# Kernel tuning notes

Hardware: AMD Instinct MI355X
Metric: run time of the kernel (lower is better)

Reference implementation:

```python
import jax, jax.numpy as jnp
import numpy as np
import math

B, S, D, H = 4, 2048, 1024, 16
DK = D // H

def setup_inputs() -> dict:
    key = jax.random.key(0)
    ks = jax.random.split(key, 6)
    scale = 1.0 / math.sqrt(D)
    x = jax.random.normal(ks[0], (B, S, D), dtype=jnp.float32)
    mask = jnp.tril(jnp.ones((S, S), dtype=jnp.int32))[None, None]  # [1,1,S,S] causal
    Wq = jax.random.normal(ks[1], (D, D), dtype=jnp.float32) * scale
    Wk = jax.random.normal(ks[2], (D, D), dtype=jnp.float32) * scale
    Wv = jax.random.normal(ks[3], (D, D), dtype=jnp.float32) * scale
    Wo = jax.random.normal(ks[4], (D, D), dtype=jnp.float32) * scale
    z = jnp.zeros((D,), dtype=jnp.float32)
    return {"x": x, "mask": mask, "Wq": Wq, "bq": z, "Wk": Wk, "bk": z,
            "Wv": Wv, "bv": z, "Wo": Wo, "bo": z}

def reference(x, mask, Wq, bq, Wk, bk, Wv, bv, Wo, bo):
    bsz, seq_len, d_model = x.shape
    def split_heads(t):  # [B,S,D] -> [B,H,S,DK]
        return t.reshape(bsz, seq_len, H, DK).transpose(0, 2, 1, 3)
    Q = split_heads(x @ Wq + bq)
    K = split_heads(x @ Wk + bk)
    V = split_heads(x @ Wv + bv)
    scores = jnp.einsum('bhqd,bhkd->bhqk', Q, K) / jnp.sqrt(jnp.asarray(DK, x.dtype))
    scores = jnp.where(mask == 0, jnp.asarray(-jnp.inf, x.dtype), scores)
    attn = jax.nn.softmax(scores, axis=-1)
    # dropout is identity in eval mode
    context = jnp.einsum('bhqk,bhkd->bhqd', attn, V)
    context = context.transpose(0, 2, 1, 3).reshape(bsz, seq_len, d_model)
    return context @ Wo + bo
```

## Files before the change

### kernel.cpp

```cpp
#include <hip/hip_runtime.h>
#include <hip/hip_bf16.h>
#include <math.h>

#define BATCH 4
#define SEQ   2048
#define DMODEL 1024
#define NHEAD 16
#define DHEAD 64
#define MROWS (BATCH * SEQ)
#define SC_Q  0.1803368801111244f

typedef __attribute__((ext_vector_type(8))) short short8;
typedef __attribute__((ext_vector_type(4))) float f32x4;
typedef __attribute__((ext_vector_type(4))) unsigned short ushort4v;

__device__ inline unsigned short f2bf(float f) {
    union { float f; unsigned int u; } v; v.f = f;
    unsigned int r = v.u + 0x7FFFu + ((v.u >> 16) & 1u);
    return (unsigned short)(r >> 16);
}
__device__ inline unsigned short f2bf_fast(float f) {
    union { float f; unsigned int u; } v; v.f = f;
    return (unsigned short)((v.u + 0x8000u) >> 16);
}

__device__ __forceinline__ void g2l16(const unsigned short* g, unsigned short* l) {
    __builtin_amdgcn_global_load_lds(
        (const __attribute__((address_space(1))) unsigned int*)g,
        (__attribute__((address_space(3))) unsigned int*)l, 16, 0, 0);
}

__global__ __launch_bounds__(256) void cvt_bf16_kernel(
    const float* __restrict__ src, unsigned short* __restrict__ dst, int n4)
{
    const int i = blockIdx.x * 256 + threadIdx.x;
    if (i < n4) {
        float4 v = ((const float4*)src)[i];
        ushort4v o = { f2bf(v.x), f2bf(v.y), f2bf(v.z), f2bf(v.w) };
        ((ushort4v*)dst)[i] = o;
    }
}

__global__ __launch_bounds__(256) void bias_pack_kernel(
    const float* __restrict__ bq, const float* __restrict__ bk,
    const float* __restrict__ bv, float* __restrict__ b3)
{
    const int i = blockIdx.x * 256 + threadIdx.x;
    if (i < DMODEL) {
        b3[i]              = bq[i];
        b3[i + DMODEL]     = bk[i];
        b3[i + 2 * DMODEL] = bv[i];
    }
}

__global__ __launch_bounds__(256) void transpose_cvt_kernel(
    const float* __restrict__ W0, const float* __restrict__ W1,
    const float* __restrict__ W2, const float* __restrict__ W3,
    unsigned short* __restrict__ T0, unsigned short* __restrict__ T1,
    unsigned short* __restrict__ T2, unsigned short* __restrict__ T3)
{
    const float* W; unsigned short* T;
    switch (blockIdx.z) {
        case 0: W = W0; T = T0; break;
        case 1: W = W1; T = T1; break;
        case 2: W = W2; T = T2; break;
        default: W = W3; T = T3; break;
    }
    __shared__ float tile[32][33];
    const int r0 = blockIdx.y * 32, c0 = blockIdx.x * 32;
    const int c = threadIdx.x & 31, r = threadIdx.x >> 5;
    #pragma unroll
    for (int i = 0; i < 4; ++i)
        tile[r + i * 8][c] = W[(size_t)(r0 + r + i * 8) * DMODEL + c0 + c];
    __syncthreads();
    #pragma unroll
    for (int i = 0; i < 4; ++i)
        T[(size_t)(c0 + r + i * 8) * DMODEL + r0 + c] = f2bf(tile[c][r + i * 8]);
}

__global__ __launch_bounds__(256) void transpose_v_kernel(
    const unsigned short* __restrict__ Vin, unsigned short* __restrict__ Vt)
{
    __shared__ unsigned short t[64][72];
    const int tid = threadIdx.x;
    const int kt = blockIdx.x, bh = blockIdx.y;
    const unsigned short* src = Vin + ((size_t)bh * SEQ + kt * 64) * DHEAD;
    const int r = tid >> 3, c = (tid & 7) * 8;
    *(short8*)&t[r][c]      = *(const short8*)(src + (size_t)r * DHEAD + c);
    *(short8*)&t[r + 32][c] = *(const short8*)(src + (size_t)(r + 32) * DHEAD + c);
    __syncthreads();
    unsigned short* dst = Vt + (size_t)bh * DHEAD * SEQ + kt * 64;
    const int d = tid >> 3, k0 = (tid & 7) * 8;
    short8 v0, v1;
    #pragma unroll
    for (int i = 0; i < 8; ++i) {
        v0[i] = (short)t[k0 + i][d];
        v1[i] = (short)t[k0 + i][d + 32];
    }
    *(short8*)(dst + (size_t)d * SEQ + k0)        = v0;
    *(short8*)(dst + (size_t)(d + 32) * SEQ + k0) = v1;
}

__global__ __launch_bounds__(256) void gemm_qkv(
    const unsigned short* __restrict__ A, const unsigned short* __restrict__ Bt,
    const float* __restrict__ bias3, unsigned short* __restrict__ QKV )
{
    __shared__ unsigned short As[128 * 32];
    __shared__ unsigned short Bs[128 * 32];

    const int tid  = threadIdx.x;
    const int wave = tid >> 6, lane = tid & 63;
    const int l15  = lane & 15, quad = lane >> 4;
    const int wm   = (wave >> 1) * 64;
    const int wn   = (wave & 1) * 64;
    const int m0   = blockIdx.y * 128;
    const int n0   = blockIdx.x * 128;
    const int Kdim = DMODEL;

    f32x4 acc[4][4];
    #pragma unroll
    for (int i = 0; i < 4; ++i)
        #pragma unroll
        for (int j = 0; j < 4; ++j) acc[i][j] = (f32x4){0.f, 0.f, 0.f, 0.f};

    const int c_lo = wave * 64 + lane;

    for (int k0 = 0; k0 < Kdim; k0 += 32) {
        __syncthreads();
        {
            int c = c_lo;
            g2l16(A  + (size_t)(m0 + (c >> 2)) * Kdim + k0 + (c & 3) * 8, As + c * 8);
            g2l16(Bt + (size_t)(n0 + (c >> 2)) * Kdim + k0 + (c & 3) * 8, Bs + c * 8);
            c = c_lo + 256;
            g2l16(A  + (size_t)(m0 + (c >> 2)) * Kdim + k0 + (c & 3) * 8, As + c * 8);
            g2l16(Bt + (size_t)(n0 + (c >> 2)) * Kdim + k0 + (c & 3) * 8, Bs + c * 8);
        }
        __syncthreads();

        short8 af[4], bf[4];
        #pragma unroll
        for (int mi = 0; mi < 4; ++mi)
            af[mi] = *(const short8*)&As[(wm + mi * 16 + l15) * 32 + quad * 8];
        #pragma unroll
        for (int ni = 0; ni < 4; ++ni)
            bf[ni] = *(const short8*)&Bs[(wn + ni * 16 + l15) * 32 + quad * 8];
        #pragma unroll
        for (int mi = 0; mi < 4; ++mi)
            #pragma unroll
            for (int ni = 0; ni < 4; ++ni)
                acc[mi][ni] = __builtin_amdgcn_mfma_f32_16x16x32_bf16(
                    af[mi], bf[ni], acc[mi][ni], 0, 0, 0);
    }

    const size_t elems = (size_t)MROWS * DMODEL;
    #pragma unroll
    for (int mi = 0; mi < 4; ++mi) {
        #pragma unroll
        for (int r = 0; r < 4; ++r) {
            const int m = m0 + wm + mi * 16 + quad * 4 + r;
            const int b = m >> 11, s = m & 2047;
            #pragma unroll
            for (int ni = 0; ni < 4; ++ni) {
                const int n   = n0 + wn + ni * 16 + l15;
                const int seg = n >> 10, nn = n & 1023;
                const int h = nn >> 6, dk = nn & 63;
                const float sc  = (seg == 0) ? SC_Q : 1.0f;
                const float val = (acc[mi][ni][r] + bias3[n]) * sc;
                QKV[seg * elems + (((size_t)(b * NHEAD + h)) * SEQ + s) * DHEAD + dk] = f2bf(val);
            }
        }
    }
}

__global__ __launch_bounds__(256) void gemm_out(
    const unsigned short* __restrict__ A, const unsigned short* __restrict__ Bt,
    const float* __restrict__ bias, float* __restrict__ Cout)
{
    __shared__ unsigned short As[128 * 32];
    __shared__ unsigned short Bs[128 * 32];

    const int tid  = threadIdx.x;
    const int wave = tid >> 6, lane = tid & 63;
    const int l15  = lane & 15, quad = lane >> 4;
    const int wm   = (wave >> 1) * 64;
    const int wn   = (wave & 1) * 64;
    const int m0   = blockIdx.y * 128;
    const int n0   = blockIdx.x * 128;
    const int Kdim = DMODEL, Ndim = DMODEL;

    f32x4 acc[4][4];
    #pragma unroll
    for (int i = 0; i < 4; ++i)
        #pragma unroll
        for (int j = 0; j < 4; ++j) acc[i][j] = (f32x4){0.f, 0.f, 0.f, 0.f};

    const int c_lo = wave * 64 + lane;

    for (int k0 = 0; k0 < Kdim; k0 += 32) {
        __syncthreads();
        {
            int c = c_lo;
            g2l16(A  + (size_t)(m0 + (c >> 2)) * Kdim + k0 + (c & 3) * 8, As + c * 8);
            g2l16(Bt + (size_t)(n0 + (c >> 2)) * Kdim + k0 + (c & 3) * 8, Bs + c * 8);
            c = c_lo + 256;
            g2l16(A  + (size_t)(m0 + (c >> 2)) * Kdim + k0 + (c & 3) * 8, As + c * 8);
            g2l16(Bt + (size_t)(n0 + (c >> 2)) * Kdim + k0 + (c & 3) * 8, Bs + c * 8);
        }
        __syncthreads();

        short8 af[4], bf[4];
        #pragma unroll
        for (int mi = 0; mi < 4; ++mi)
            af[mi] = *(const short8*)&As[(wm + mi * 16 + l15) * 32 + quad * 8];
        #pragma unroll
        for (int ni = 0; ni < 4; ++ni)
            bf[ni] = *(const short8*)&Bs[(wn + ni * 16 + l15) * 32 + quad * 8];
        #pragma unroll
        for (int mi = 0; mi < 4; ++mi)
            #pragma unroll
            for (int ni = 0; ni < 4; ++ni)
                acc[mi][ni] = __builtin_amdgcn_mfma_f32_16x16x32_bf16(
                    af[mi], bf[ni], acc[mi][ni], 0, 0, 0);
    }

    #pragma unroll
    for (int mi = 0; mi < 4; ++mi) {
        #pragma unroll
        for (int r = 0; r < 4; ++r) {
            const int m = m0 + wm + mi * 16 + quad * 4 + r;
            #pragma unroll
            for (int ni = 0; ni < 4; ++ni) {
                const int n = n0 + wn + ni * 16 + l15;
                Cout[(size_t)m * Ndim + n] = acc[mi][ni][r] + bias[n];
            }
        }
    }
}

__global__ __launch_bounds__(256, 3) void attn_mfma4(
    const unsigned short* __restrict__ Q, const unsigned short* __restrict__ K,
    const unsigned short* __restrict__ VtG, unsigned short* __restrict__ ctx_out)
{
    __shared__ alignas(16) unsigned short Ks[64 * 64];
    __shared__ alignas(16) unsigned short Vts[64 * 64];
    __shared__ alignas(16) unsigned short Ps[4][32][72];

    const int tid  = threadIdx.x;
    const int wave = tid >> 6, lane = tid & 63;
    const int l15  = lane & 15, quad = lane >> 4;
    const int qa   = blockIdx.x;
    const int qb   = 31 - qa;
    const int bh   = blockIdx.y;
    const int b    = bh >> 4, h = bh & 15;

    const unsigned short* Kb0 = K   + (size_t)bh * SEQ * DHEAD;
    const unsigned short* Vb0 = VtG + (size_t)bh * DHEAD * SEQ;

    short8 qf[2][2];
    #pragma unroll
    for (int g = 0; g < 2; ++g) {
        const int qtile = g ? qb : qa;
        const unsigned short* qrow = Q + ((size_t)bh * SEQ + qtile * 64 + wave * 16 + l15) * DHEAD + quad * 8;
        qf[g][0] = *(const short8*)qrow;
        qf[g][1] = *(const short8*)(qrow + 32);
    }

    f32x4 Of[2][4];
    float l_r[2][4];
    #pragma unroll
    for (int g = 0; g < 2; ++g)
        #pragma unroll
        for (int i = 0; i < 4; ++i) { Of[g][i] = (f32x4){0.f,0.f,0.f,0.f}; l_r[g][i] = 0.f; }

    const int jb_end  = qb;
    const int row_loc = wave * 16 + quad * 4;
    const f32x4 zero4 = (f32x4){0.f, 0.f, 0.f, 0.f};

    const int c0c = wave * 64 + lane;
    short8 kreg[2], vreg[2];

    #pragma unroll
    for (int i = 0; i < 2; ++i) {
        const int c = c0c + i * 256;
        const int k = c >> 3, qs = c & 7;
        const int gq = qs ^ (k & 7);
        kreg[i] = *(const short8*)(Kb0 + (size_t)k * DHEAD + gq * 8);
        vreg[i] = *(const short8*)(Vb0 + (size_t)k * SEQ   + gq * 8);
    }

    for (int jb = 0; jb <= jb_end; ++jb) {
        __syncthreads();
        #pragma unroll
        for (int i = 0; i < 2; ++i) {
            const int c = c0c + i * 256;
            *(short8*)&Ks[c * 8]  = kreg[i];
            *(short8*)&Vts[c * 8] = vreg[i];
        }
        if (jb < jb_end) {
            const unsigned short* Kt  = Kb0 + (size_t)(jb + 1) * 64 * DHEAD;
            const unsigned short* Vt0 = Vb0 + (jb + 1) * 64;
            #pragma unroll
            for (int i = 0; i < 2; ++i) {
                const int c = c0c + i * 256;
                const int k = c >> 3, qs = c & 7;
                const int gq = qs ^ (k & 7);
                kreg[i] = *(const short8*)(Kt  + (size_t)k * DHEAD + gq * 8);
                vreg[i] = *(const short8*)(Vt0 + (size_t)k * SEQ   + gq * 8);
            }
        }
        __syncthreads();

        const bool act0  = (jb <= qa);
        const bool diag0 = (jb == qa);
        const bool diag1 = (jb == qb);

        #pragma unroll
        for (int nt = 0; nt < 4; ++nt) {
            const int k = nt * 16 + l15;
            short8 b0 = *(const short8*)&Ks[(k * 8 + ( quad      ^ (k & 7))) * 8];
            short8 b1 = *(const short8*)&Ks[(k * 8 + ((quad + 4) ^ (k & 7))) * 8];
            const int col = nt * 16 + l15;

            f32x4 s1 = __builtin_amdgcn_mfma_f32_16x16x32_bf16(qf[1][0], b0, zero4, 0, 0, 0);
            s1       = __builtin_amdgcn_mfma_f32_16x16x32_bf16(qf[1][1], b1, s1,    0, 0, 0);
            #pragma unroll
            for (int r = 0; r < 4; ++r) {
                float p = __builtin_amdgcn_exp2f(s1[r]);
                if (diag1 && col > row_loc + r) p = 0.f;
                l_r[1][r] += p;
                Ps[wave][16 + quad * 4 + r][col] = f2bf_fast(p);
            }
            if (act0) {
                f32x4 s0 = __builtin_amdgcn_mfma_f32_16x16x32_bf16(qf[0][0], b0, zero4, 0, 0, 0);
                s0       = __builtin_amdgcn_mfma_f32_16x16x32_bf16(qf[0][1], b1, s0,    0, 0, 0);
                #pragma unroll
                for (int r = 0; r < 4; ++r) {
                    float p = __builtin_amdgcn_exp2f(s0[r]);
                    if (diag0 && col > row_loc + r) p = 0.f;
                    l_r[0][r] += p;
                    Ps[wave][quad * 4 + r][col] = f2bf_fast(p);
                }
            }
        }

        short8 pa1_0 = *(const short8*)&Ps[wave][16 + l15][quad * 8];
        short8 pa1_1 = *(const short8*)&Ps[wave][16 + l15][32 + quad * 8];
        short8 pa0_0, pa0_1;
        if (act0) {
            pa0_0 = *(const short8*)&Ps[wave][l15][quad * 8];
            pa0_1 = *(const short8*)&Ps[wave][l15][32 + quad * 8];
        }
        #pragma unroll
        for (int nt = 0; nt < 4; ++nt) {
            const int d = nt * 16 + l15;
            short8 vb0 = *(const short8*)&Vts[(d * 8 + ( quad      ^ (d & 7))) * 8];
            short8 vb1 = *(const short8*)&Vts[(d * 8 + ((quad + 4) ^ (d & 7))) * 8];
            Of[1][nt] = __builtin_amdgcn_mfma_f32_16x16x32_bf16(pa1_0, vb0, Of[1][nt], 0, 0, 0);
            Of[1][nt] = __builtin_amdgcn_mfma_f32_16x16x32_bf16(pa1_1, vb1, Of[1][nt], 0, 0, 0);
            if (act0) {
                Of[0][nt] = __builtin_amdgcn_mfma_f32_16x16x32_bf16(pa0_0, vb0, Of[0][nt], 0, 0, 0);
                Of[0][nt] = __builtin_amdgcn_mfma_f32_16x16x32_bf16(pa0_1, vb1, Of[0][nt], 0, 0, 0);
            }
        }
    }

    #pragma unroll
    for (int g = 0; g < 2; ++g) {
        const int qtile = g ? qb : qa;
        #pragma unroll
        for (int r = 0; r < 4; ++r) {
            float l = l_r[g][r];
            l += __shfl_xor(l, 1);
            l += __shfl_xor(l, 2);
            l += __shfl_xor(l, 4);
            l += __shfl_xor(l, 8);
            const float inv = 1.0f / l;
            const int s = qtile * 64 + wave * 16 + quad * 4 + r;
            unsigned short* o = ctx_out + ((size_t)(b * SEQ + s)) * DMODEL + h * DHEAD;
            #pragma unroll
            for (int nt = 0; nt < 4; ++nt)
                o[nt * 16 + l15] = f2bf(Of[g][nt][r] * inv);
        }
    }
}

extern "C" void kernel_launch(void* const* d_in, const int* in_sizes, int n_in,
                              void* d_out, int out_size, void* d_ws, size_t ws_size,
                              hipStream_t stream) {
    const float* x  = (const float*)d_in[0];
    const float* Wq = (const float*)d_in[2];
    const float* bq = (const float*)d_in[3];
    const float* Wk = (const float*)d_in[4];
    const float* bk = (const float*)d_in[5];
    const float* Wv = (const float*)d_in[6];
    const float* bv = (const float*)d_in[7];
    const float* Wo = (const float*)d_in[8];
    const float* bo = (const float*)d_in[9];
    float* out = (float*)d_out;

    const size_t elems  = (size_t)MROWS * DMODEL;
    const size_t welems = (size_t)DMODEL * DMODEL;
    unsigned short* xbf   = (unsigned short*)d_ws;
    unsigned short* WqkvT = xbf + elems;
    unsigned short* WoT   = WqkvT + 3 * welems;
    unsigned short* Qbuf  = WoT + welems;
    unsigned short* Kbuf  = Qbuf + elems;
    unsigned short* Vbuf  = Kbuf + elems;
    unsigned short* VtG   = Vbuf + elems;
    unsigned short* Cbuf  = VtG + elems;
    float*          bias3 = (float*)(Cbuf + elems);

    dim3 blk(256);

    cvt_bf16_kernel<<<dim3((int)(elems / 4 / 256)), blk, 0, stream>>>(x, xbf, (int)(elems / 4));
    transpose_cvt_kernel<<<dim3(32, 32, 4), blk, 0, stream>>>(
        Wq, Wk, Wv, Wo, WqkvT, WqkvT + welems, WqkvT + 2 * welems, WoT);
    bias_pack_kernel<<<dim3(4), blk, 0, stream>>>(bq, bk, bv, bias3);

    dim3 gqkv(3 * DMODEL / 128, MROWS / 128);
    gemm_qkv<<<gqkv, blk, 0, stream>>>(xbf, WqkvT, bias3, Qbuf);

    transpose_v_kernel<<<dim3(SEQ / 64, BATCH * NHEAD), blk, 0, stream>>>(Vbuf, VtG);

    dim3 gattn(16, BATCH * NHEAD);
    attn_mfma4<<<gattn, blk, 0, stream>>>(Qbuf, Kbuf, VtG, Cbuf);

    dim3 gout(DMODEL / 128, MROWS / 128);
    gemm_out<<<gout, blk, 0, stream>>>(Cbuf, WoT, bo, out);
}
```

Measured before the change: 319.1 us.

## Compute S transposed to keep P in registers and drop LDS round-trip

The attention kernel now computes S^T (K as the A operand, Q as B) so each lane's exp'd probabilities already sit in the register layout needed as the A operand of a 16x16x16 bf16 MFMA for P·V. This removes the per-wave Ps shared-memory staging buffer and its stores and loads. The packed bf16 conversion now uses v_cvt_pk_bf16_f32. The kernel also drops the paired q-tile load balancing in favour of one q-tile per block with a 32-wide grid and launch bounds raised to 8 blocks per CU. This gives more, smaller blocks with uneven causal work, and moves the prefetch of the next K/V tile to after the QK step.

```diff
diff --git a/kernel.cpp b/kernel.cpp
--- a/kernel.cpp
+++ b/kernel.cpp
@@ -11,6 +11,7 @@
 #define SC_Q  0.1803368801111244f
 
 typedef __attribute__((ext_vector_type(8))) short short8;
+typedef __attribute__((ext_vector_type(4))) short short4_t;
 typedef __attribute__((ext_vector_type(4))) float f32x4;
 typedef __attribute__((ext_vector_type(4))) unsigned short ushort4v;
 
@@ -19,9 +20,11 @@
     unsigned int r = v.u + 0x7FFFu + ((v.u >> 16) & 1u);
     return (unsigned short)(r >> 16);
 }
-__device__ inline unsigned short f2bf_fast(float f) {
-    union { float f; unsigned int u; } v; v.f = f;
-    return (unsigned short)((v.u + 0x8000u) >> 16);
+
+__device__ inline unsigned int cvt_pk_bf16(float a, float b) {
+    unsigned int r;
+    asm("v_cvt_pk_bf16_f32 %0, %1, %2" : "=v"(r) : "v"(a), "v"(b));
+    return r;
 }
 
 __device__ __forceinline__ void g2l16(const unsigned short* g, unsigned short* l) {
@@ -237,150 +240,117 @@
     }
 }
 
-__global__ __launch_bounds__(256, 3) void attn_mfma4(
+__global__ __launch_bounds__(256, 8) void attn_mfma5(
     const unsigned short* __restrict__ Q, const unsigned short* __restrict__ K,
     const unsigned short* __restrict__ VtG, unsigned short* __restrict__ ctx_out)
 {
     __shared__ alignas(16) unsigned short Ks[64 * 64];
     __shared__ alignas(16) unsigned short Vts[64 * 64];
-    __shared__ alignas(16) unsigned short Ps[4][32][72];
 
     const int tid  = threadIdx.x;
     const int wave = tid >> 6, lane = tid & 63;
     const int l15  = lane & 15, quad = lane >> 4;
-    const int qa   = blockIdx.x;
-    const int qb   = 31 - qa;
+    const int qi   = 31 - blockIdx.x;
     const int bh   = blockIdx.y;
     const int b    = bh >> 4, h = bh & 15;
 
     const unsigned short* Kb0 = K   + (size_t)bh * SEQ * DHEAD;
     const unsigned short* Vb0 = VtG + (size_t)bh * DHEAD * SEQ;
 
-    short8 qf[2][2];
-    #pragma unroll
-    for (int g = 0; g < 2; ++g) {
-        const int qtile = g ? qb : qa;
-        const unsigned short* qrow = Q + ((size_t)bh * SEQ + qtile * 64 + wave * 16 + l15) * DHEAD + quad * 8;
-        qf[g][0] = *(const short8*)qrow;
-        qf[g][1] = *(const short8*)(qrow + 32);
-    }
-
-    f32x4 Of[2][4];
-    float l_r[2][4];
-    #pragma unroll
-    for (int g = 0; g < 2; ++g)
-        #pragma unroll
-        for (int i = 0; i < 4; ++i) { Of[g][i] = (f32x4){0.f,0.f,0.f,0.f}; l_r[g][i] = 0.f; }
-
-    const int jb_end  = qb;
-    const int row_loc = wave * 16 + quad * 4;
+    const unsigned short* qrow =
+        Q + ((size_t)bh * SEQ + qi * 64 + wave * 16 + l15) * DHEAD + quad * 8;
+    const short8 qf0 = *(const short8*)qrow;
+    const short8 qf1 = *(const short8*)(qrow + 32);
+
+    f32x4 Of[4];
+    #pragma unroll
+    for (int i = 0; i < 4; ++i) Of[i] = (f32x4){0.f, 0.f, 0.f, 0.f};
+    float lsum = 0.f;
+    const int qloc = wave * 16 + l15;
     const f32x4 zero4 = (f32x4){0.f, 0.f, 0.f, 0.f};
 
-    const int c0c = wave * 64 + lane;
     short8 kreg[2], vreg[2];
-
     #pragma unroll
     for (int i = 0; i < 2; ++i) {
-        const int c = c0c + i * 256;
-        const int k = c >> 3, qs = c & 7;
-        const int gq = qs ^ (k & 7);
-        kreg[i] = *(const short8*)(Kb0 + (size_t)k * DHEAD + gq * 8);
-        vreg[i] = *(const short8*)(Vb0 + (size_t)k * SEQ   + gq * 8);
-    }
-
-    for (int jb = 0; jb <= jb_end; ++jb) {
+        const int c = tid + i * 256;
+        const int kk = c >> 3, qs = c & 7;
+        const int gq = qs ^ (kk & 7);
+        kreg[i] = *(const short8*)(Kb0 + (size_t)kk * DHEAD + gq * 8);
+        vreg[i] = *(const short8*)(Vb0 + (size_t)kk * SEQ   + gq * 8);
+    }
+
+    for (int jb = 0; jb <= qi; ++jb) {
         __syncthreads();
         #pragma unroll
         for (int i = 0; i < 2; ++i) {
-            const int c = c0c + i * 256;
+            const int c = tid + i * 256;
             *(short8*)&Ks[c * 8]  = kreg[i];
             *(short8*)&Vts[c * 8] = vreg[i];
         }
-        if (jb < jb_end) {
+        __syncthreads();
+
+        const bool diag = (jb == qi);
+
+        short4_t pw[4];
+        #pragma unroll
+        for (int nt = 0; nt < 4; ++nt) {
+            const int k = nt * 16 + l15;
+            const short8 a0 = *(const short8*)&Ks[(k * 8 + ( quad      ^ (k & 7))) * 8];
+            const short8 a1 = *(const short8*)&Ks[(k * 8 + ((quad + 4) ^ (k & 7))) * 8];
+            f32x4 s = __builtin_amdgcn_mfma_f32_16x16x32_bf16(a0, qf0, zero4, 0, 0, 0);
+            s       = __builtin_amdgcn_mfma_f32_16x16x32_bf16(a1, qf1, s,     0, 0, 0);
+            f32x4 p;
+            #pragma unroll
+            for (int r = 0; r < 4; ++r) p[r] = __builtin_amdgcn_exp2f(s[r]);
+            if (diag) {
+                #pragma unroll
+                for (int r = 0; r < 4; ++r)
+                    if (nt * 16 + quad * 4 + r > qloc) p[r] = 0.f;
+            }
+            lsum += (p[0] + p[1]) + (p[2] + p[3]);
+            union { unsigned int u[2]; short4_t v; } pk;
+            pk.u[0] = cvt_pk_bf16(p[0], p[1]);
+            pk.u[1] = cvt_pk_bf16(p[2], p[3]);
+            pw[nt] = pk.v;
+        }
+
+        if (jb < qi) {
             const unsigned short* Kt  = Kb0 + (size_t)(jb + 1) * 64 * DHEAD;
             const unsigned short* Vt0 = Vb0 + (jb + 1) * 64;
             #pragma unroll
             for (int i = 0; i < 2; ++i) {
-                const int c = c0c + i * 256;
-                const int k = c >> 3, qs = c & 7;
-                const int gq = qs ^ (k & 7);
-                kreg[i] = *(const short8*)(Kt  + (size_t)k * DHEAD + gq * 8);
-                vreg[i] = *(const short8*)(Vt0 + (size_t)k * SEQ   + gq * 8);
+                const int c = tid + i * 256;
+                const int kk = c >> 3, qs = c & 7;
+                const int gq = qs ^ (kk & 7);
+                kreg[i] = *(const short8*)(Kt  + (size_t)kk * DHEAD + gq * 8);
+                vreg[i] = *(const short8*)(Vt0 + (size_t)kk * SEQ   + gq * 8);
             }
         }
-        __syncthreads();
-
-        const bool act0  = (jb <= qa);
-        const bool diag0 = (jb == qa);
-        const bool diag1 = (jb == qb);
-
-        #pragma unroll
-        for (int nt = 0; nt < 4; ++nt) {
-            const int k = nt * 16 + l15;
-            short8 b0 = *(const short8*)&Ks[(k * 8 + ( quad      ^ (k & 7))) * 8];
-            short8 b1 = *(const short8*)&Ks[(k * 8 + ((quad + 4) ^ (k & 7))) * 8];
-            const int col = nt * 16 + l15;
-
-            f32x4 s1 = __builtin_amdgcn_mfma_f32_16x16x32_bf16(qf[1][0], b0, zero4, 0, 0, 0);
-            s1       = __builtin_amdgcn_mfma_f32_16x16x32_bf16(qf[1][1], b1, s1,    0, 0, 0);
-            #pragma unroll
-            for (int r = 0; r < 4; ++r) {
-                float p = __builtin_amdgcn_exp2f(s1[r]);
-                if (diag1 && col > row_loc + r) p = 0.f;
-                l_r[1][r] += p;
-                Ps[wave][16 + quad * 4 + r][col] = f2bf_fast(p);
+
+        #pragma unroll
+        for (int kc = 0; kc < 4; ++kc) {
+            #pragma unroll
+            for (int nt = 0; nt < 4; ++nt) {
+                const int d  = nt * 16 + l15;
+                const int kb = kc * 2 + (quad >> 1);
+                const short4_t vb = *(const short4_t*)
+                    &Vts[(d * 8 + (kb ^ (d & 7))) * 8 + (quad & 1) * 4];
+                Of[nt] = __builtin_amdgcn_mfma_f32_16x16x16bf16_1k(
+                    pw[kc], vb, Of[nt], 0, 0, 0);
             }
-            if (act0) {
-                f32x4 s0 = __builtin_amdgcn_mfma_f32_16x16x32_bf16(qf[0][0], b0, zero4, 0, 0, 0);
-                s0       = __builtin_amdgcn_mfma_f32_16x16x32_bf16(qf[0][1], b1, s0,    0, 0, 0);
-                #pragma unroll
-                for (int r = 0; r < 4; ++r) {
-                    float p = __builtin_amdgcn_exp2f(s0[r]);
-                    if (diag0 && col > row_loc + r) p = 0.f;
-                    l_r[0][r] += p;
-                    Ps[wave][quad * 4 + r][col] = f2bf_fast(p);
-                }
-            }
-        }
-
-        short8 pa1_0 = *(const short8*)&Ps[wave][16 + l15][quad * 8];
-        short8 pa1_1 = *(const short8*)&Ps[wave][16 + l15][32 + quad * 8];
-        short8 pa0_0, pa0_1;
-        if (act0) {
-            pa0_0 = *(const short8*)&Ps[wave][l15][quad * 8];
-            pa0_1 = *(const short8*)&Ps[wave][l15][32 + quad * 8];
-        }
-        #pragma unroll
-        for (int nt = 0; nt < 4; ++nt) {
-            const int d = nt * 16 + l15;
-            short8 vb0 = *(const short8*)&Vts[(d * 8 + ( quad      ^ (d & 7))) * 8];
-            short8 vb1 = *(const short8*)&Vts[(d * 8 + ((quad + 4) ^ (d & 7))) * 8];
-            Of[1][nt] = __builtin_amdgcn_mfma_f32_16x16x32_bf16(pa1_0, vb0, Of[1][nt], 0, 0, 0);
-            Of[1][nt] = __builtin_amdgcn_mfma_f32_16x16x32_bf16(pa1_1, vb1, Of[1][nt], 0, 0, 0);
-            if (act0) {
-                Of[0][nt] = __builtin_amdgcn_mfma_f32_16x16x32_bf16(pa0_0, vb0, Of[0][nt], 0, 0, 0);
-                Of[0][nt] = __builtin_amdgcn_mfma_f32_16x16x32_bf16(pa0_1, vb1, Of[0][nt], 0, 0, 0);
-            }
-        }
-    }
-
-    #pragma unroll
-    for (int g = 0; g < 2; ++g) {
-        const int qtile = g ? qb : qa;
-        #pragma unroll
-        for (int r = 0; r < 4; ++r) {
-            float l = l_r[g][r];
-            l += __shfl_xor(l, 1);
-            l += __shfl_xor(l, 2);
-            l += __shfl_xor(l, 4);
-            l += __shfl_xor(l, 8);
-            const float inv = 1.0f / l;
-            const int s = qtile * 64 + wave * 16 + quad * 4 + r;
-            unsigned short* o = ctx_out + ((size_t)(b * SEQ + s)) * DMODEL + h * DHEAD;
-            #pragma unroll
-            for (int nt = 0; nt < 4; ++nt)
-                o[nt * 16 + l15] = f2bf(Of[g][nt][r] * inv);
-        }
+        }
+    }
+
+    lsum += __shfl_xor(lsum, 16);
+    lsum += __shfl_xor(lsum, 32);
+    #pragma unroll
+    for (int r = 0; r < 4; ++r) {
+        const float inv = 1.0f / __shfl(lsum, quad * 4 + r);
+        const int s = qi * 64 + wave * 16 + quad * 4 + r;
+        unsigned short* o = ctx_out + ((size_t)(b * SEQ + s)) * DMODEL + h * DHEAD;
+        #pragma unroll
+        for (int nt = 0; nt < 4; ++nt)
+            o[nt * 16 + l15] = f2bf(Of[nt][r] * inv);
     }
 }
 
@@ -422,8 +392,8 @@
 
     transpose_v_kernel<<<dim3(SEQ / 64, BATCH * NHEAD), blk, 0, stream>>>(Vbuf, VtG);
 
-    dim3 gattn(16, BATCH * NHEAD);
-    attn_mfma4<<<gattn, blk, 0, stream>>>(Qbuf, Kbuf, VtG, Cbuf);
+    dim3 gattn(32, BATCH * NHEAD);
+    attn_mfma5<<<gattn, blk, 0, stream>>>(Qbuf, Kbuf, VtG, Cbuf);
 
     dim3 gout(DMODEL / 128, MROWS / 128);
     gemm_out<<<gout, blk, 0, stream>>>(Cbuf, WoT, bo, out);
```

After: 658.5 us. +106.3%, slower.
